# Kernel tuning notes

Hardware: AMD Instinct MI355X
Metric: run time of the kernel (lower is better)

Reference implementation:

```python
import jax, jax.numpy as jnp
import numpy as np
from functools import partial

SAMPLE_RATE = 48000
BITRATE = 128000
M = 1024            # AAC_FRAME_LENGTH (hop, MDCT bins)
N = 2048            # AAC_WINDOW_LENGTH
TARGET_BITS = BITRATE * M / SAMPLE_RATE   # bits per frame (all channels)
MAX_GAIN = 120.0
EPS = 1e-9


def _window():
    # sine window satisfies Princen-Bradley: w[n]^2 + w[n+M]^2 = 1
    n = jnp.arange(N, dtype=jnp.float32)
    return jnp.sin(jnp.pi / N * (n + 0.5))


def _cosmat():
    # MDCT basis  C[n,k] = cos(pi/M (n + 0.5 + M/2)(k + 0.5)),  shape (N, M)
    n = jnp.arange(N, dtype=jnp.float32)[:, None]
    k = jnp.arange(M, dtype=jnp.float32)[None, :]
    return jnp.cos(jnp.pi / M * (n + 0.5 + M / 2) * (k + 0.5))


def _frame_bits(ax75, gain):
    """Estimated coded bits per frame under hard AAC power-law quantization.
    ax75: |coeff|^{3/4}, shape (B,F,C,M); gain: (B,F)."""
    inv = jnp.exp2(-0.75 * gain / 4.0)[:, :, None, None]
    qmag = jnp.round(ax75 * inv)
    # sign-magnitude style cost: nonzero -> floor(log2|q|)+2 bits, zero -> 1 bit
    bits = jnp.where(qmag > 0.0,
                     jnp.floor(jnp.log2(jnp.maximum(qmag, 1.0))) + 2.0,
                     1.0)
    return jnp.sum(bits, axis=(2, 3))  # (B,F)


def _find_global_gain(coeffs_bfcm):
    """Integer binary search for smallest gain with bits <= TARGET_BITS. (no grad)"""
    ax75 = jnp.abs(jax.lax.stop_gradient(coeffs_bfcm)) ** 0.75
    B, F = ax75.shape[0], ax75.shape[1]
    lo = jnp.zeros((B, F), jnp.float32)
    hi = jnp.full((B, F), MAX_GAIN, jnp.float32)

    def body(_, carry):
        lo, hi = carry
        mid = jnp.floor((lo + hi) / 2.0)
        too_big = _frame_bits(ax75, mid) > TARGET_BITS
        lo = jnp.where(too_big, mid + 1.0, lo)
        hi = jnp.where(too_big, hi, mid)
        return lo, hi

    _, hi = jax.lax.fori_loop(0, 8, body, (lo, hi))  # 8 iters covers [0,120]
    return hi  # (B,F)


def reference(audio):
    B, C, T = audio.shape
    w = _window()
    Cm = _cosmat()

    # --- frame_audio: left-pad M, right-pad to full frames ---
    F = -(-(T + M) // M)
    pad_right = F * M + M - (T + M)
    x = jnp.pad(audio, ((0, 0), (0, 0), (M, pad_right)))
    idx = jnp.arange(F)[:, None] * M + jnp.arange(N)[None, :]      # (F,N)
    frames = x[:, :, idx]                                          # (B,C,F,N)

    # --- analysis window + MDCT ---
    windowed = frames * w
    coeffs = jnp.einsum('bcfn,nk->bcfk', windowed, Cm)             # (B,C,F,M)
    coeffs_bfcm = jnp.transpose(coeffs, (0, 2, 1, 3))              # (B,F,C,M)

    # --- iterative global-gain search (hard quant, no grad) ---
    gains = _find_global_gain(coeffs_bfcm)                         # (B,F)

    # --- quantize (STE) / dequantize: q = round((|x| 2^{-g/4})^{3/4}) ---
    scale = jnp.exp2(gains / 4.0)[:, :, None, None]
    sgn = jnp.sign(coeffs_bfcm)
    q_soft = sgn * (jnp.abs(coeffs_bfcm) / scale + EPS) ** 0.75
    q = q_soft + jax.lax.stop_gradient(jnp.round(q_soft) - q_soft)
    dq = jnp.sign(q) * jnp.abs(q) ** (4.0 / 3.0) * scale           # (B,F,C,M)

    # --- IMDCT + synthesis window ---
    dq_bcfm = jnp.transpose(dq, (0, 2, 1, 3))                      # (B,C,F,M)
    td = (2.0 / M) * jnp.einsum('bcfk,nk->bcfn', dq_bcfm, Cm)      # (B,C,F,N)
    rew = td * w

    # --- overlap-add (hop M) ---
    out = jnp.zeros((B, C, (F + 1) * M), audio.dtype)
    out = out.at[:, :, :F * M].add(rew[:, :, :, :M].reshape(B, C, F * M))
    out = out.at[:, :, M:].add(rew[:, :, :, M:].reshape(B, C, F * M))
    return out[:, :, M:M + T]


def setup_inputs() -> dict:
    key = jax.random.key(0)
    audio = 0.5 * jax.random.normal(key, (8, 2, 1440000), dtype=jnp.float32)
    return {"audio": audio}
```

## Files before the change

kernel.cpp:

```cpp
#include <hip/hip_runtime.h>
#include <math.h>

#define B_ 8
#define C_ 2
#define T_ 1440000
#define F_ 1408
#define R_ 22528
#define TARGET_HI 2731

#define OFF_CFH 0ull
#define OFF_CFL (4ull << 20)
#define OFF_CIH (8ull << 20)
#define OFF_WF  (12ull << 20)
#define OFF_CF  (13ull << 20)
#define OFF_DQ  (OFF_CF + (size_t)R_ * 1024 * 4)

typedef _Float16 f16x8 __attribute__((ext_vector_type(8)));
typedef _Float16 f16x4 __attribute__((ext_vector_type(4)));
typedef float f32x16 __attribute__((ext_vector_type(16)));

__device__ inline f32x16 mfma16(f16x8 a, f16x8 b, f32x16 c) {
  return __builtin_amdgcn_mfma_f32_32x32x16_f16(a, b, c, 0, 0, 0);
}

__device__ inline void gld_lds16(const void* g, void* l) {
  __builtin_amdgcn_global_load_lds(
      (const __attribute__((address_space(1))) void*)g,
      (__attribute__((address_space(3))) void*)l, 16, 0, 0);
}

__global__ __launch_bounds__(256) void init_tables(char* wsb) {
  _Float16* cfh = (_Float16*)(wsb + OFF_CFH);
  _Float16* cfl = (_Float16*)(wsb + OFF_CFL);
  _Float16* cih = (_Float16*)(wsb + OFF_CIH);
  float*    wf  = (float*)(wsb + OFF_WF);
  int idx = blockIdx.x * 256 + threadIdx.x;
  if (idx < 2097152) {
    int n = idx >> 10, k = idx & 1023;
    const float c0 = (float)(M_PI / 1024.0);
    float a  = (float)n + 0.5f + 512.0f;
    float t1 = c0 * a;
    float ph = t1 * ((float)k + 0.5f);
    float cm = (float)cos((double)ph);
    _Float16 h = (_Float16)cm;
    _Float16 l = (_Float16)(cm - (float)h);
    cfh[(size_t)k * 2048 + n] = h;
    cfl[(size_t)k * 2048 + n] = l;
    cih[(size_t)n * 1024 + k] = h;
  } else if (idx < 2097152 + 2048) {
    int n = idx - 2097152;
    const float c1 = (float)(M_PI / 2048.0);
    float ph = c1 * ((float)n + 0.5f);
    wf[n] = (float)sin((double)ph);
  }
}

__global__ __launch_bounds__(256) void fwd_mfma(const float* __restrict__ audio,
                                                const char* __restrict__ wsb,
                                                float* __restrict__ coeffs) {
  __shared__ _Float16 Ah[128][40];
  __shared__ _Float16 Al[128][40];
  __shared__ _Float16 Bh[128][40];
  __shared__ _Float16 Bl[128][40];
  const _Float16* cfh = (const _Float16*)(wsb + OFF_CFH);
  const _Float16* cfl = (const _Float16*)(wsb + OFF_CFL);
  const float*    wf  = (const float*)(wsb + OFF_WF);

  int tid = threadIdx.x;
  int lane = tid & 63, wid = tid >> 6;
  int l31 = lane & 31, lHalf = lane >> 5;
  int waveM = wid >> 1, waveN = wid & 1;
  int rowTile = blockIdx.x * 128, colTile = blockIdx.y * 128;

  int sRow = tid >> 1;
  int sSeg = (tid & 1) << 4;
  int r = rowTile + sRow, bc = r / F_, f = r - bc * F_;
  const float* __restrict__ aud = audio + (size_t)bc * T_;
  int tBase = (f << 10) - 1024 + sSeg;
  const _Float16* bhp = cfh + (size_t)(colTile + sRow) * 2048 + sSeg;
  const _Float16* blp = cfl + (size_t)(colTile + sRow) * 2048 + sSeg;

  f32x16 acc[2][2];
#pragma unroll
  for (int i = 0; i < 2; i++)
#pragma unroll
    for (int j = 0; j < 2; j++)
#pragma unroll
      for (int e = 0; e < 16; e++) acc[i][j][e] = 0.f;

  for (int kt = 0; kt < 2048; kt += 32) {
    float av[16];
    int t0 = tBase + kt;
    if (t0 >= 0 && t0 + 16 <= T_) {
#pragma unroll
      for (int q = 0; q < 4; q++) {
        float4 x = *(const float4*)(aud + t0 + q * 4);
        av[q * 4 + 0] = x.x; av[q * 4 + 1] = x.y;
        av[q * 4 + 2] = x.z; av[q * 4 + 3] = x.w;
      }
    } else {
#pragma unroll
      for (int i = 0; i < 16; i++) {
        int t = t0 + i;
        av[i] = (t >= 0 && t < T_) ? aud[t] : 0.f;
      }
    }
    f16x8 vh[2], vl[2];
#pragma unroll
    for (int i = 0; i < 16; i++) {
      float v = av[i] * wf[kt + sSeg + i];
      _Float16 h = (_Float16)v;
      vh[i >> 3][i & 7] = h;
      vl[i >> 3][i & 7] = (_Float16)(v - (float)h);
    }
    float4 tb0 = *(const float4*)(bhp + kt);
    float4 tb1 = *(const float4*)(bhp + kt + 8);
    float4 tl0 = *(const float4*)(blp + kt);
    float4 tl1 = *(const float4*)(blp + kt + 8);

    __syncthreads();
    *(f16x8*)&Ah[sRow][sSeg]     = vh[0];
    *(f16x8*)&Ah[sRow][sSeg + 8] = vh[1];
    *(f16x8*)&Al[sRow][sSeg]     = vl[0];
    *(f16x8*)&Al[sRow][sSeg + 8] = vl[1];
    *(float4*)&Bh[sRow][sSeg]     = tb0;
    *(float4*)&Bh[sRow][sSeg + 8] = tb1;
    *(float4*)&Bl[sRow][sSeg]     = tl0;
    *(float4*)&Bl[sRow][sSeg + 8] = tl1;
    __syncthreads();

#pragma unroll
    for (int kc = 0; kc < 2; kc++) {
      int ko = kc * 16 + lHalf * 8;
      f16x8 a_h[2], a_l[2], b_h[2], b_l[2];
#pragma unroll
      for (int mi = 0; mi < 2; mi++) {
        a_h[mi] = *(const f16x8*)&Ah[waveM * 64 + mi * 32 + l31][ko];
        a_l[mi] = *(const f16x8*)&Al[waveM * 64 + mi * 32 + l31][ko];
      }
#pragma unroll
      for (int ni = 0; ni < 2; ni++) {
        b_h[ni] = *(const f16x8*)&Bh[waveN * 64 + ni * 32 + l31][ko];
        b_l[ni] = *(const f16x8*)&Bl[waveN * 64 + ni * 32 + l31][ko];
      }
#pragma unroll
      for (int mi = 0; mi < 2; mi++)
#pragma unroll
        for (int ni = 0; ni < 2; ni++) {
          acc[mi][ni] = mfma16(a_h[mi], b_h[ni], acc[mi][ni]);
          acc[mi][ni] = mfma16(a_h[mi], b_l[ni], acc[mi][ni]);
          acc[mi][ni] = mfma16(a_l[mi], b_h[ni], acc[mi][ni]);
        }
    }
  }

#pragma unroll
  for (int mi = 0; mi < 2; mi++)
#pragma unroll
    for (int ni = 0; ni < 2; ni++) {
      int col = colTile + waveN * 64 + ni * 32 + l31;
#pragma unroll
      for (int reg = 0; reg < 16; reg++) {
        int rowIn = (reg & 3) + 8 * (reg >> 2) + 4 * lHalf;
        int rr = rowTile + waveM * 64 + mi * 32 + rowIn;
        coeffs[(size_t)rr * 1024 + col] = acc[mi][ni][reg];
      }
    }
}

__global__ __launch_bounds__(256) void quantize(const float* __restrict__ cf,
                                                _Float16* __restrict__ dqh) {
  int wid = threadIdx.x >> 6, lane = threadIdx.x & 63;
  int bf = blockIdx.x * 4 + wid;
  int b = bf / F_, f = bf - b * F_;
  size_t base0 = ((size_t)(b * C_ + 0) * F_ + f) * 1024;
  size_t base1 = ((size_t)(b * C_ + 1) * F_ + f) * 1024;

  float x[32], ax75[32];
#pragma unroll
  for (int c = 0; c < 2; c++) {
    size_t bb = c ? base1 : base0;
#pragma unroll
    for (int j = 0; j < 4; j++) {
      float4 v = *(const float4*)(cf + bb + j * 256 + lane * 4);
      int o = c * 16 + j * 4;
      x[o + 0] = v.x; x[o + 1] = v.y; x[o + 2] = v.z; x[o + 3] = v.w;
    }
  }
#pragma unroll
  for (int u = 0; u < 32; u++) {
    float ax = fabsf(x[u]);
    float s  = sqrtf(ax);
    ax75[u]  = s * sqrtf(s);
  }

  int lo = 0, hi = 120;
#pragma unroll
  for (int it = 0; it < 8; it++) {
    int mid = (lo + hi) >> 1;
    float inv = exp2f(-0.1875f * (float)mid);
    int s = 0;
#pragma unroll
    for (int u = 0; u < 32; u++) {
      float qm = rintf(ax75[u] * inv);
      int iq = (int)qm;
      s += (iq > 0) ? (33 - __clz(iq)) : 1;
    }
#pragma unroll
    for (int off = 1; off < 64; off <<= 1) s += __shfl_xor(s, off, 64);
    if (s >= TARGET_HI) lo = mid + 1; else hi = mid;
  }

  float scale = exp2f(0.25f * (float)hi);
  float rs    = exp2f(-0.25f * (float)hi);
#pragma unroll
  for (int c = 0; c < 2; c++) {
    size_t bb = c ? base1 : base0;
#pragma unroll
    for (int j = 0; j < 4; j++) {
      f16x4 o4;
#pragma unroll
      for (int e = 0; e < 4; e++) {
        int u = c * 16 + j * 4 + e;
        float ax  = fabsf(x[u]);
        float t   = ax * rs + 1e-9f;
        float s1  = sqrtf(t);
        float qs  = s1 * sqrtf(s1);
        float q   = rintf(qs);
        float q43 = q * exp2f(__log2f(q) * (1.0f / 3.0f));
        o4[e] = (_Float16)copysignf(q43 * scale, x[u]);
      }
      *(f16x4*)(dqh + bb + j * 256 + lane * 4) = o4;
    }
  }
}

__global__ __launch_bounds__(256) void inv_mfma(const char* __restrict__ wsb,
                                               float* __restrict__ out) {
  __shared__ _Float16 Ad[128][64];
  __shared__ _Float16 Bd[256][64];
  const _Float16* dqh = (const _Float16*)(wsb + OFF_DQ);
  const _Float16* cih = (const _Float16*)(wsb + OFF_CIH);
  const float*    wf  = (const float*)(wsb + OFF_WF);

  int tid = threadIdx.x;
  int lane = tid & 63, wid = tid >> 6;
  int l31 = lane & 31, lHalf = lane >> 5;
  int waveM = wid >> 1, waveN = wid & 1;
  int rowTile = blockIdx.x * 128, colTile = blockIdx.y * 256;

  int srcRowOff = lane >> 3;
  int swz8 = ((lane & 7) ^ (lane >> 3)) << 3;
  const _Float16* aSrc = dqh + (size_t)(rowTile + wid * 32 + srcRowOff) * 1024 + swz8;
  const _Float16* bSrc = cih + (size_t)(colTile + wid * 64 + srcRowOff) * 1024 + swz8;

  f32x16 acc[2][4];
#pragma unroll
  for (int i = 0; i < 2; i++)
#pragma unroll
    for (int j = 0; j < 4; j++)
#pragma unroll
      for (int e = 0; e < 16; e++) acc[i][j][e] = 0.f;

  int xoru = l31 & 7;
  const char* adB = (const char*)&Ad[0][0];
  const char* bdB = (const char*)&Bd[0][0];
  int arow0 = (waveM * 64 + l31) << 7;
  int brow0 = (waveN * 128 + l31) << 7;

  for (int kt = 0; kt < 1024; kt += 64) {
    __syncthreads();
#pragma unroll
    for (int i = 0; i < 4; i++)
      gld_lds16(aSrc + kt + (size_t)i * 8192, &Ad[wid * 32 + i * 8][0]);
#pragma unroll
    for (int i = 0; i < 8; i++)
      gld_lds16(bSrc + kt + (size_t)i * 8192, &Bd[wid * 64 + i * 8][0]);
    asm volatile("s_waitcnt vmcnt(0)" ::: "memory");
    __syncthreads();

#pragma unroll
    for (int kc = 0; kc < 4; kc++) {
      int su = (((kc * 2 + lHalf) ^ xoru) << 4);
      f16x8 a0 = *(const f16x8*)(adB + arow0 + su);
      f16x8 a1 = *(const f16x8*)(adB + arow0 + 32 * 128 + su);
      f16x8 b0 = *(const f16x8*)(bdB + brow0 + su);
      f16x8 b1 = *(const f16x8*)(bdB + brow0 + 32 * 128 + su);
      f16x8 b2 = *(const f16x8*)(bdB + brow0 + 64 * 128 + su);
      f16x8 b3 = *(const f16x8*)(bdB + brow0 + 96 * 128 + su);
      acc[0][0] = mfma16(a0, b0, acc[0][0]);
      acc[0][1] = mfma16(a0, b1, acc[0][1]);
      acc[0][2] = mfma16(a0, b2, acc[0][2]);
      acc[0][3] = mfma16(a0, b3, acc[0][3]);
      acc[1][0] = mfma16(a1, b0, acc[1][0]);
      acc[1][1] = mfma16(a1, b1, acc[1][1]);
      acc[1][2] = mfma16(a1, b2, acc[1][2]);
      acc[1][3] = mfma16(a1, b3, acc[1][3]);
    }
  }

  const float sc = 2.0f / 1024.0f;
#pragma unroll
  for (int mi = 0; mi < 2; mi++)
#pragma unroll
    for (int ni = 0; ni < 4; ni++) {
      int n = colTile + waveN * 128 + ni * 32 + l31;
      float wv = wf[n] * sc;
#pragma unroll
      for (int reg = 0; reg < 16; reg++) {
        int rowIn = (reg & 3) + 8 * (reg >> 2) + 4 * lHalf;
        int rr = rowTile + waveM * 64 + mi * 32 + rowIn;
        int bc = rr / F_;
        int f  = rr - bc * F_;
        int t  = (f << 10) + n - 1024;
        if (t >= 0 && t < T_)
          unsafeAtomicAdd(out + (size_t)bc * T_ + t, acc[mi][ni][reg] * wv);
      }
    }
}

extern "C" void kernel_launch(void* const* d_in, const int* in_sizes, int n_in,
                              void* d_out, int out_size, void* d_ws, size_t ws_size,
                              hipStream_t stream) {
  const float* audio = (const float*)d_in[0];
  float* out = (float*)d_out;
  char* wsb  = (char*)d_ws;
  float*    cf  = (float*)(wsb + OFF_CF);
  _Float16* dqh = (_Float16*)(wsb + OFF_DQ);

  hipMemsetAsync(d_out, 0, (size_t)out_size * sizeof(float), stream);
  init_tables<<<(2097152 + 2048 + 255) / 256, 256, 0, stream>>>(wsb);
  fwd_mfma<<<dim3(R_ / 128, 1024 / 128), 256, 0, stream>>>(audio, wsb, cf);
  quantize<<<(B_ * F_) / 4, 256, 0, stream>>>(cf, dqh);
  inv_mfma<<<dim3(R_ / 128, 2048 / 256), 256, 0, stream>>>(wsb, out);
}
```

Before: 838.7 us.

## Double-buffer LDS tiles in forward and inverse MDCT GEMMs with async B loads

Both MFMA GEMM kernels now keep two LDS buffers and prefetch the next K-tile while computing on the current one, so each iteration needs one barrier instead of two. In the forward kernel the cosine-basis tiles move from register-staged loads to direct global-to-LDS loads with an XOR swizzle, and the window values are loaded as vectors. The inverse kernel shrinks its K-tile from 64 to 32 to fit two buffers, which doubles the number of barrier iterations. LDS use per block grows, which may lower occupancy.

Result: slower. 998.6 us (+19.1%).

```diff
diff --git a/kernel.cpp b/kernel.cpp
--- a/kernel.cpp
+++ b/kernel.cpp
@@ -58,10 +58,10 @@
 __global__ __launch_bounds__(256) void fwd_mfma(const float* __restrict__ audio,
                                                 const char* __restrict__ wsb,
                                                 float* __restrict__ coeffs) {
-  __shared__ _Float16 Ah[128][40];
-  __shared__ _Float16 Al[128][40];
-  __shared__ _Float16 Bh[128][40];
-  __shared__ _Float16 Bl[128][40];
+  __shared__ _Float16 Ah[2][128][40];
+  __shared__ _Float16 Al[2][128][40];
+  __shared__ __align__(16) _Float16 Bh[2][128][32];
+  __shared__ __align__(16) _Float16 Bl[2][128][32];
   const _Float16* cfh = (const _Float16*)(wsb + OFF_CFH);
   const _Float16* cfl = (const _Float16*)(wsb + OFF_CFL);
   const float*    wf  = (const float*)(wsb + OFF_WF);
@@ -77,8 +77,11 @@
   int r = rowTile + sRow, bc = r / F_, f = r - bc * F_;
   const float* __restrict__ aud = audio + (size_t)bc * T_;
   int tBase = (f << 10) - 1024 + sSeg;
-  const _Float16* bhp = cfh + (size_t)(colTile + sRow) * 2048 + sSeg;
-  const _Float16* blp = cfl + (size_t)(colTile + sRow) * 2048 + sSeg;
+
+  int srcRow = lane >> 2;
+  int swz = ((lane & 3) ^ (srcRow & 3)) << 3;
+  const _Float16* bhS = cfh + (size_t)(colTile + wid * 32 + srcRow) * 2048 + swz;
+  const _Float16* blS = cfl + (size_t)(colTile + wid * 32 + srcRow) * 2048 + swz;
 
   f32x16 acc[2][2];
 #pragma unroll
@@ -88,8 +91,9 @@
 #pragma unroll
       for (int e = 0; e < 16; e++) acc[i][j][e] = 0.f;
 
-  for (int kt = 0; kt < 2048; kt += 32) {
-    float av[16];
+  float av[16], wv[16];
+
+  auto loadA = [&](int kt) {
     int t0 = tBase + kt;
     if (t0 >= 0 && t0 + 16 <= T_) {
 #pragma unroll
@@ -105,43 +109,62 @@
         av[i] = (t >= 0 && t < T_) ? aud[t] : 0.f;
       }
     }
+#pragma unroll
+    for (int q = 0; q < 4; q++)
+      *(float4*)&wv[q * 4] = *(const float4*)(wf + kt + sSeg + q * 4);
+  };
+
+  auto stageB = [&](int kt, int buf) {
+    gld_lds16(bhS + kt,             &Bh[buf][wid * 32][0]);
+    gld_lds16(bhS + kt + 16 * 2048, &Bh[buf][wid * 32 + 16][0]);
+    gld_lds16(blS + kt,             &Bl[buf][wid * 32][0]);
+    gld_lds16(blS + kt + 16 * 2048, &Bl[buf][wid * 32 + 16][0]);
+  };
+
+  auto writeA = [&](int buf) {
     f16x8 vh[2], vl[2];
 #pragma unroll
     for (int i = 0; i < 16; i++) {
-      float v = av[i] * wf[kt + sSeg + i];
+      float v = av[i] * wv[i];
       _Float16 h = (_Float16)v;
       vh[i >> 3][i & 7] = h;
       vl[i >> 3][i & 7] = (_Float16)(v - (float)h);
     }
-    float4 tb0 = *(const float4*)(bhp + kt);
-    float4 tb1 = *(const float4*)(bhp + kt + 8);
-    float4 tl0 = *(const float4*)(blp + kt);
-    float4 tl1 = *(const float4*)(blp + kt + 8);
-
-    __syncthreads();
-    *(f16x8*)&Ah[sRow][sSeg]     = vh[0];
-    *(f16x8*)&Ah[sRow][sSeg + 8] = vh[1];
-    *(f16x8*)&Al[sRow][sSeg]     = vl[0];
-    *(f16x8*)&Al[sRow][sSeg + 8] = vl[1];
-    *(float4*)&Bh[sRow][sSeg]     = tb0;
-    *(float4*)&Bh[sRow][sSeg + 8] = tb1;
-    *(float4*)&Bl[sRow][sSeg]     = tl0;
-    *(float4*)&Bl[sRow][sSeg + 8] = tl1;
-    __syncthreads();
-
+    *(f16x8*)&Ah[buf][sRow][sSeg]     = vh[0];
+    *(f16x8*)&Ah[buf][sRow][sSeg + 8] = vh[1];
+    *(f16x8*)&Al[buf][sRow][sSeg]     = vl[0];
+    *(f16x8*)&Al[buf][sRow][sSeg + 8] = vl[1];
+  };
+
+  loadA(0);
+  stageB(0, 0);
+  writeA(0);
+  asm volatile("s_waitcnt vmcnt(0)" ::: "memory");
+  __syncthreads();
+
+  int cur = 0;
+  for (int kt = 0; kt < 2048; kt += 32) {
+    bool more = (kt + 32) < 2048;
+    if (more) {
+      loadA(kt + 32);
+      stageB(kt + 32, cur ^ 1);
+    }
 #pragma unroll
     for (int kc = 0; kc < 2; kc++) {
       int ko = kc * 16 + lHalf * 8;
+      int slot = ((kc * 2 + lHalf) ^ (l31 & 3)) << 4;
       f16x8 a_h[2], a_l[2], b_h[2], b_l[2];
 #pragma unroll
       for (int mi = 0; mi < 2; mi++) {
-        a_h[mi] = *(const f16x8*)&Ah[waveM * 64 + mi * 32 + l31][ko];
-        a_l[mi] = *(const f16x8*)&Al[waveM * 64 + mi * 32 + l31][ko];
+        a_h[mi] = *(const f16x8*)&Ah[cur][waveM * 64 + mi * 32 + l31][ko];
+        a_l[mi] = *(const f16x8*)&Al[cur][waveM * 64 + mi * 32 + l31][ko];
       }
 #pragma unroll
       for (int ni = 0; ni < 2; ni++) {
-        b_h[ni] = *(const f16x8*)&Bh[waveN * 64 + ni * 32 + l31][ko];
-        b_l[ni] = *(const f16x8*)&Bl[waveN * 64 + ni * 32 + l31][ko];
+        const char* bp = (const char*)&Bh[cur][waveN * 64 + ni * 32 + l31][0];
+        const char* bq = (const char*)&Bl[cur][waveN * 64 + ni * 32 + l31][0];
+        b_h[ni] = *(const f16x8*)(bp + slot);
+        b_l[ni] = *(const f16x8*)(bq + slot);
       }
 #pragma unroll
       for (int mi = 0; mi < 2; mi++)
@@ -152,6 +175,10 @@
           acc[mi][ni] = mfma16(a_l[mi], b_h[ni], acc[mi][ni]);
         }
     }
+    if (more) writeA(cur ^ 1);
+    asm volatile("s_waitcnt vmcnt(0)" ::: "memory");
+    __syncthreads();
+    cur ^= 1;
   }
 
 #pragma unroll
@@ -237,8 +264,8 @@
 
 __global__ __launch_bounds__(256) void inv_mfma(const char* __restrict__ wsb,
                                                float* __restrict__ out) {
-  __shared__ _Float16 Ad[128][64];
-  __shared__ _Float16 Bd[256][64];
+  __shared__ __align__(16) _Float16 Ad[2][128][32];
+  __shared__ __align__(16) _Float16 Bd[2][256][32];
   const _Float16* dqh = (const _Float16*)(wsb + OFF_DQ);
   const _Float16* cih = (const _Float16*)(wsb + OFF_CIH);
   const float*    wf  = (const float*)(wsb + OFF_WF);
@@ -249,10 +276,18 @@
   int waveM = wid >> 1, waveN = wid & 1;
   int rowTile = blockIdx.x * 128, colTile = blockIdx.y * 256;
 
-  int srcRowOff = lane >> 3;
-  int swz8 = ((lane & 7) ^ (lane >> 3)) << 3;
-  const _Float16* aSrc = dqh + (size_t)(rowTile + wid * 32 + srcRowOff) * 1024 + swz8;
-  const _Float16* bSrc = cih + (size_t)(colTile + wid * 64 + srcRowOff) * 1024 + swz8;
+  int srcRow = lane >> 2;
+  int swz = ((lane & 3) ^ (srcRow & 3)) << 3;
+  const _Float16* aS = dqh + (size_t)(rowTile + wid * 32 + srcRow) * 1024 + swz;
+  const _Float16* bS = cih + (size_t)(colTile + wid * 64 + srcRow) * 1024 + swz;
+
+  auto stage = [&](int kt, int buf) {
+    gld_lds16(aS + kt,             &Ad[buf][wid * 32][0]);
+    gld_lds16(aS + kt + 16 * 1024, &Ad[buf][wid * 32 + 16][0]);
+#pragma unroll
+    for (int j = 0; j < 4; j++)
+      gld_lds16(bS + kt + (size_t)j * 16 * 1024, &Bd[buf][wid * 64 + j * 16][0]);
+  };
 
   f32x16 acc[2][4];
 #pragma unroll
@@ -262,32 +297,24 @@
 #pragma unroll
       for (int e = 0; e < 16; e++) acc[i][j][e] = 0.f;
 
-  int xoru = l31 & 7;
-  const char* adB = (const char*)&Ad[0][0];
-  const char* bdB = (const char*)&Bd[0][0];
-  int arow0 = (waveM * 64 + l31) << 7;
-  int brow0 = (waveN * 128 + l31) << 7;
-
-  for (int kt = 0; kt < 1024; kt += 64) {
-    __syncthreads();
-#pragma unroll
-    for (int i = 0; i < 4; i++)
-      gld_lds16(aSrc + kt + (size_t)i * 8192, &Ad[wid * 32 + i * 8][0]);
-#pragma unroll
-    for (int i = 0; i < 8; i++)
-      gld_lds16(bSrc + kt + (size_t)i * 8192, &Bd[wid * 64 + i * 8][0]);
-    asm volatile("s_waitcnt vmcnt(0)" ::: "memory");
-    __syncthreads();
-
-#pragma unroll
-    for (int kc = 0; kc < 4; kc++) {
-      int su = (((kc * 2 + lHalf) ^ xoru) << 4);
-      f16x8 a0 = *(const f16x8*)(adB + arow0 + su);
-      f16x8 a1 = *(const f16x8*)(adB + arow0 + 32 * 128 + su);
-      f16x8 b0 = *(const f16x8*)(bdB + brow0 + su);
-      f16x8 b1 = *(const f16x8*)(bdB + brow0 + 32 * 128 + su);
-      f16x8 b2 = *(const f16x8*)(bdB + brow0 + 64 * 128 + su);
-      f16x8 b3 = *(const f16x8*)(bdB + brow0 + 96 * 128 + su);
+  stage(0, 0);
+  asm volatile("s_waitcnt vmcnt(0)" ::: "memory");
+  __syncthreads();
+
+  int cur = 0;
+  for (int kt = 0; kt < 1024; kt += 32) {
+    if (kt + 32 < 1024) stage(kt + 32, cur ^ 1);
+#pragma unroll
+    for (int kc = 0; kc < 2; kc++) {
+      int slot = ((kc * 2 + lHalf) ^ (l31 & 3)) << 4;
+      const char* ar = (const char*)&Ad[cur][waveM * 64 + l31][0];
+      const char* br = (const char*)&Bd[cur][waveN * 128 + l31][0];
+      f16x8 a0 = *(const f16x8*)(ar + slot);
+      f16x8 a1 = *(const f16x8*)(ar + 32 * 64 + slot);
+      f16x8 b0 = *(const f16x8*)(br + slot);
+      f16x8 b1 = *(const f16x8*)(br + 32 * 64 + slot);
+      f16x8 b2 = *(const f16x8*)(br + 64 * 64 + slot);
+      f16x8 b3 = *(const f16x8*)(br + 96 * 64 + slot);
       acc[0][0] = mfma16(a0, b0, acc[0][0]);
       acc[0][1] = mfma16(a0, b1, acc[0][1]);
       acc[0][2] = mfma16(a0, b2, acc[0][2]);
@@ -297,6 +324,9 @@
       acc[1][2] = mfma16(a1, b2, acc[1][2]);
       acc[1][3] = mfma16(a1, b3, acc[1][3]);
     }
+    asm volatile("s_waitcnt vmcnt(0)" ::: "memory");
+    __syncthreads();
+    cur ^= 1;
   }
 
   const float sc = 2.0f / 1024.0f;
```

## Replace atomic overlap-add with fp16 frame buffer and separate OLA kernel

Applied to the files above, without the earlier changes.

The inverse MDCT GEMM no longer scatters windowed results into the output with float atomics. It writes the windowed time-domain frames as fp16 into a workspace buffer that reuses the coefficient region. A new elementwise kernel then sums the two overlapping halves and writes the output with vectorized stores, so the output memset is no longer needed. The GEMM K loop also changes from a single 64-wide buffer to a double-buffered 32-wide tile with a new swizzle, overlapping the global-to-LDS loads with MFMA work. The cost is an extra kernel launch, a large fp16 intermediate write and read, and fp16 rounding of the time-domain frames before the sum.

Result: faster. 798.1 us (-4.8%).

```diff
diff --git a/kernel.cpp b/kernel.cpp
--- a/kernel.cpp
+++ b/kernel.cpp
@@ -235,10 +235,10 @@
   }
 }
 
-__global__ __launch_bounds__(256) void inv_mfma(const char* __restrict__ wsb,
-                                               float* __restrict__ out) {
-  __shared__ _Float16 Ad[128][64];
-  __shared__ _Float16 Bd[256][64];
+__global__ __launch_bounds__(256) void inv_gemm(const char* __restrict__ wsb,
+                                                _Float16* __restrict__ tdh) {
+  __shared__ __align__(16) _Float16 Ad[2][128][32];
+  __shared__ __align__(16) _Float16 Bd[2][256][32];
   const _Float16* dqh = (const _Float16*)(wsb + OFF_DQ);
   const _Float16* cih = (const _Float16*)(wsb + OFF_CIH);
   const float*    wf  = (const float*)(wsb + OFF_WF);
@@ -249,10 +249,18 @@
   int waveM = wid >> 1, waveN = wid & 1;
   int rowTile = blockIdx.x * 128, colTile = blockIdx.y * 256;
 
-  int srcRowOff = lane >> 3;
-  int swz8 = ((lane & 7) ^ (lane >> 3)) << 3;
-  const _Float16* aSrc = dqh + (size_t)(rowTile + wid * 32 + srcRowOff) * 1024 + swz8;
-  const _Float16* bSrc = cih + (size_t)(colTile + wid * 64 + srcRowOff) * 1024 + swz8;
+  int srcRow = lane >> 2;
+  int swz = ((lane & 3) ^ ((lane >> 3) & 3)) << 3;
+  const _Float16* aS = dqh + (size_t)(rowTile + wid * 32 + srcRow) * 1024 + swz;
+  const _Float16* bS = cih + (size_t)(colTile + wid * 64 + srcRow) * 1024 + swz;
+
+  auto stage = [&](int kt, int buf) {
+    gld_lds16(aS + kt,             &Ad[buf][wid * 32][0]);
+    gld_lds16(aS + kt + 16 * 1024, &Ad[buf][wid * 32 + 16][0]);
+#pragma unroll
+    for (int j = 0; j < 4; j++)
+      gld_lds16(bS + kt + (size_t)j * 16 * 1024, &Bd[buf][wid * 64 + j * 16][0]);
+  };
 
   f32x16 acc[2][4];
 #pragma unroll
@@ -262,32 +270,24 @@
 #pragma unroll
       for (int e = 0; e < 16; e++) acc[i][j][e] = 0.f;
 
-  int xoru = l31 & 7;
-  const char* adB = (const char*)&Ad[0][0];
-  const char* bdB = (const char*)&Bd[0][0];
-  int arow0 = (waveM * 64 + l31) << 7;
-  int brow0 = (waveN * 128 + l31) << 7;
-
-  for (int kt = 0; kt < 1024; kt += 64) {
-    __syncthreads();
-#pragma unroll
-    for (int i = 0; i < 4; i++)
-      gld_lds16(aSrc + kt + (size_t)i * 8192, &Ad[wid * 32 + i * 8][0]);
-#pragma unroll
-    for (int i = 0; i < 8; i++)
-      gld_lds16(bSrc + kt + (size_t)i * 8192, &Bd[wid * 64 + i * 8][0]);
-    asm volatile("s_waitcnt vmcnt(0)" ::: "memory");
-    __syncthreads();
-
-#pragma unroll
-    for (int kc = 0; kc < 4; kc++) {
-      int su = (((kc * 2 + lHalf) ^ xoru) << 4);
-      f16x8 a0 = *(const f16x8*)(adB + arow0 + su);
-      f16x8 a1 = *(const f16x8*)(adB + arow0 + 32 * 128 + su);
-      f16x8 b0 = *(const f16x8*)(bdB + brow0 + su);
-      f16x8 b1 = *(const f16x8*)(bdB + brow0 + 32 * 128 + su);
-      f16x8 b2 = *(const f16x8*)(bdB + brow0 + 64 * 128 + su);
-      f16x8 b3 = *(const f16x8*)(bdB + brow0 + 96 * 128 + su);
+  stage(0, 0);
+  asm volatile("s_waitcnt vmcnt(0)" ::: "memory");
+  __syncthreads();
+
+  int cur = 0;
+  for (int kt = 0; kt < 1024; kt += 32) {
+    if (kt + 32 < 1024) stage(kt + 32, cur ^ 1);
+#pragma unroll
+    for (int kc = 0; kc < 2; kc++) {
+      int slot = ((kc * 2 + lHalf) ^ ((l31 >> 1) & 3)) << 4;
+      const char* ar = (const char*)&Ad[cur][waveM * 64 + l31][0];
+      const char* br = (const char*)&Bd[cur][waveN * 128 + l31][0];
+      f16x8 a0 = *(const f16x8*)(ar + slot);
+      f16x8 a1 = *(const f16x8*)(ar + 32 * 64 + slot);
+      f16x8 b0 = *(const f16x8*)(br + slot);
+      f16x8 b1 = *(const f16x8*)(br + 32 * 64 + slot);
+      f16x8 b2 = *(const f16x8*)(br + 64 * 64 + slot);
+      f16x8 b3 = *(const f16x8*)(br + 96 * 64 + slot);
       acc[0][0] = mfma16(a0, b0, acc[0][0]);
       acc[0][1] = mfma16(a0, b1, acc[0][1]);
       acc[0][2] = mfma16(a0, b2, acc[0][2]);
@@ -297,6 +297,9 @@
       acc[1][2] = mfma16(a1, b2, acc[1][2]);
       acc[1][3] = mfma16(a1, b3, acc[1][3]);
     }
+    asm volatile("s_waitcnt vmcnt(0)" ::: "memory");
+    __syncthreads();
+    cur ^= 1;
   }
 
   const float sc = 2.0f / 1024.0f;
@@ -310,13 +313,33 @@
       for (int reg = 0; reg < 16; reg++) {
         int rowIn = (reg & 3) + 8 * (reg >> 2) + 4 * lHalf;
         int rr = rowTile + waveM * 64 + mi * 32 + rowIn;
-        int bc = rr / F_;
-        int f  = rr - bc * F_;
-        int t  = (f << 10) + n - 1024;
-        if (t >= 0 && t < T_)
-          unsafeAtomicAdd(out + (size_t)bc * T_ + t, acc[mi][ni][reg] * wv);
-      }
-    }
+        tdh[(size_t)rr * 2048 + n] = (_Float16)(acc[mi][ni][reg] * wv);
+      }
+    }
+}
+
+__global__ __launch_bounds__(256) void ola(const char* __restrict__ wsb,
+                                           float* __restrict__ out) {
+  const _Float16* tdh = (const _Float16*)(wsb + OFF_CF);
+  int idx = blockIdx.x * 256 + threadIdx.x;
+  size_t base = (size_t)idx * 8;
+  int bc = (int)(base / T_);
+  int t  = (int)(base - (size_t)bc * T_);
+  int g = t >> 10, o = t & 1023;
+  size_t r0 = (size_t)bc * F_ + g;
+  f16x8 hi = *(const f16x8*)(tdh + (r0 + 1) * 2048 + o);
+  f16x8 lo = *(const f16x8*)(tdh + r0 * 2048 + 1024 + o);
+  float4 v0, v1;
+  v0.x = (float)hi[0] + (float)lo[0];
+  v0.y = (float)hi[1] + (float)lo[1];
+  v0.z = (float)hi[2] + (float)lo[2];
+  v0.w = (float)hi[3] + (float)lo[3];
+  v1.x = (float)hi[4] + (float)lo[4];
+  v1.y = (float)hi[5] + (float)lo[5];
+  v1.z = (float)hi[6] + (float)lo[6];
+  v1.w = (float)hi[7] + (float)lo[7];
+  *(float4*)(out + base)     = v0;
+  *(float4*)(out + base + 4) = v1;
 }
 
 extern "C" void kernel_launch(void* const* d_in, const int* in_sizes, int n_in,
@@ -327,10 +350,11 @@
   char* wsb  = (char*)d_ws;
   float*    cf  = (float*)(wsb + OFF_CF);
   _Float16* dqh = (_Float16*)(wsb + OFF_DQ);
-
-  hipMemsetAsync(d_out, 0, (size_t)out_size * sizeof(float), stream);
+  _Float16* tdh = (_Float16*)(wsb + OFF_CF);
+
   init_tables<<<(2097152 + 2048 + 255) / 256, 256, 0, stream>>>(wsb);
   fwd_mfma<<<dim3(R_ / 128, 1024 / 128), 256, 0, stream>>>(audio, wsb, cf);
   quantize<<<(B_ * F_) / 4, 256, 0, stream>>>(cf, dqh);
-  inv_mfma<<<dim3(R_ / 128, 2048 / 256), 256, 0, stream>>>(wsb, out);
-}
+  inv_gemm<<<dim3(R_ / 128, 2048 / 256), 256, 0, stream>>>(wsb, tdh);
+  ola<<<(B_ * C_ * T_) / (256 * 8), 256, 0, stream>>>(wsb, out);
+}
```
